# Performance work log

Hardware: AMD Instinct MI355X
Metric: run time of the kernel (lower is better)

The kernel has to match this reference:

```python
import jax, jax.numpy as jnp
import numpy as np

N = 50000; E = 800000; F_IN = 128; H = 16; G = 256
DIMS = [F_IN, H, 2 * H, 4 * H, 4 * H, 8 * H]
EPS = 1e-5


def setup_inputs() -> dict:
    key = jax.random.key(0)
    ks = iter(jax.random.split(key, 40))
    inp = {}
    inp["x"] = jax.random.normal(next(ks), (N, F_IN), dtype=jnp.float32)
    inp["edge_index"] = jax.random.randint(next(ks), (2, E), 0, N, dtype=jnp.int32)
    inp["edge_weight"] = jax.random.uniform(next(ks), (E,), dtype=jnp.float32)
    inp["batch"] = jnp.sort(jax.random.randint(next(ks), (N,), 0, G, dtype=jnp.int32))
    for i in range(5):
        din, dout = DIMS[i], DIMS[i + 1]
        inp[f"W{i+1}"] = jax.random.normal(next(ks), (din, dout), dtype=jnp.float32) / np.sqrt(din).astype(np.float32)
        inp[f"b{i+1}"] = jnp.zeros((dout,), jnp.float32)
        inp[f"g{i+1}"] = jnp.ones((dout,), jnp.float32)
        inp[f"bt{i+1}"] = jnp.zeros((dout,), jnp.float32)
    inp["fc1_w"] = jax.random.normal(next(ks), (8 * H, 4 * H), dtype=jnp.float32) / np.sqrt(8 * H).astype(np.float32)
    inp["fc1_b"] = jnp.zeros((4 * H,), jnp.float32)
    inp["fc2_w"] = jax.random.normal(next(ks), (4 * H, 1), dtype=jnp.float32) / np.sqrt(4 * H).astype(np.float32)
    inp["fc2_b"] = jnp.zeros((1,), jnp.float32)
    return inp


def _gcn_norm(edge_index, edge_weight, n):
    # PyG GCNConv: add self-loops (weight 1), symmetric deg^-1/2 normalization.
    loop = jnp.arange(n, dtype=edge_index.dtype)
    row = jnp.concatenate([edge_index[0], loop])  # source
    col = jnp.concatenate([edge_index[1], loop])  # target
    w = jnp.concatenate([edge_weight, jnp.ones((n,), edge_weight.dtype)])
    deg = jax.ops.segment_sum(w, col, num_segments=n)
    dis = jnp.where(deg > 0, jax.lax.rsqrt(jnp.maximum(deg, 1e-12)), 0.0)
    return row, col, dis[row] * w * dis[col]


def _bn(h, g, b):
    # BatchNorm1d, training-mode batch statistics (biased variance, eps=1e-5)
    mu = h.mean(0)
    v = h.var(0)
    return g * (h - mu) * jax.lax.rsqrt(v + EPS) + b


def reference(x, edge_index, edge_weight, batch,
              W1, b1, g1, bt1, W2, b2, g2, bt2, W3, b3, g3, bt3,
              W4, b4, g4, bt4, W5, b5, g5, bt5,
              fc1_w, fc1_b, fc2_w, fc2_b):
    n = x.shape[0]
    row, col, norm = _gcn_norm(edge_index, edge_weight, n)

    def conv(h, W, b):
        m = h @ W                                   # [N, dout] dense transform
        agg = jax.ops.segment_sum(m[row] * norm[:, None], col, num_segments=n)
        return agg + b

    h = _bn(jax.nn.relu(conv(x, W1, b1)), g1, bt1)
    h = _bn(jax.nn.relu(conv(h, W2, b2)), g2, bt2)
    h = _bn(jax.nn.relu(conv(h, W3, b3)), g3, bt3)
    h = jax.nn.relu(_bn(conv(h, W4, b4), g4, bt4))   # layer4: conv->bn->relu
    h = _bn(conv(h, W5, b5), g5, bt5)                # layer5: conv->bn
    pooled = jax.ops.segment_sum(h, batch, num_segments=G)  # global_add_pool -> [G, 8H]
    p = jax.nn.relu(pooled)
    p = jax.nn.relu(p @ fc1_w + fc1_b)
    # dropout is identity in eval mode
    return (p @ fc2_w + fc2_b).reshape(-1)          # [G]
```

## Files before the change

### kernel.cpp

```cpp
#include <hip/hip_runtime.h>
#include <stdint.h>

#define NN 50000
#define NE 800000
#define NG 256
#define NBUCKET 16
#define PARTSZ (NBUCKET * 256)

#define NBKT 391
#define ABLK 391
#define ASLICE 2048
#define BCAP 2560

__device__ __forceinline__ float bf2f(unsigned short u) {
    return __uint_as_float(((unsigned)u) << 16);
}
__device__ __forceinline__ unsigned short f2bf(float f) {
    unsigned b = __float_as_uint(f);
    return (unsigned short)((b + 0x7FFF + ((b >> 16) & 1)) >> 16);
}

__global__ void kA1(const int* __restrict__ col, int* __restrict__ bb, float* part, int e) {
    __shared__ int cnt[NBKT];
    for (int j = threadIdx.x; j < NBKT; j += 256) cnt[j] = 0;
    for (int i = blockIdx.x * 256 + threadIdx.x; i < 5 * PARTSZ; i += ABLK * 256) part[i] = 0.f;
    __syncthreads();
    int start = blockIdx.x * ASLICE;
    int end = min(start + ASLICE, e);
    for (int i = start + threadIdx.x; i < end; i += 256)
        atomicAdd(&cnt[col[i] >> 7], 1);
    __syncthreads();
    for (int j = threadIdx.x; j < NBKT; j += 256) bb[blockIdx.x * NBKT + j] = cnt[j];
}

__global__ void kA2a(int* __restrict__ bb, int* __restrict__ totals) {
    __shared__ int v[ABLK];
    int k = blockIdx.x;
    for (int b = threadIdx.x; b < ABLK; b += 256) v[b] = bb[b * NBKT + k];
    __syncthreads();
    if (threadIdx.x == 0) {
        int run = 0;
        for (int b = 0; b < ABLK; ++b) { int t = v[b]; v[b] = run; run += t; }
        totals[k] = run;
    }
    __syncthreads();
    for (int b = threadIdx.x; b < ABLK; b += 256) bb[b * NBKT + k] = v[b];
}

__global__ void kA2b(const int* __restrict__ totals, int* __restrict__ bucketbase) {
    __shared__ int v[NBKT];
    for (int j = threadIdx.x; j < NBKT; j += 256) v[j] = totals[j];
    __syncthreads();
    if (threadIdx.x == 0) {
        int run = 0;
        for (int k = 0; k < NBKT; ++k) { int t = v[k]; v[k] = run; run += t; }
        bucketbase[NBKT] = run;
    }
    __syncthreads();
    for (int j = threadIdx.x; j < NBKT; j += 256) bucketbase[j] = v[j];
}

__global__ void kA3(const int* __restrict__ row, const int* __restrict__ col,
                    const float* __restrict__ ew, const int* __restrict__ bb,
                    const int* __restrict__ bucketbase, int2* __restrict__ staging, int e) {
    __shared__ int cur[NBKT];
    for (int j = threadIdx.x; j < NBKT; j += 256)
        cur[j] = bucketbase[j] + bb[blockIdx.x * NBKT + j];
    __syncthreads();
    int start = blockIdx.x * ASLICE;
    int end = min(start + ASLICE, e);
    for (int i = start + threadIdx.x; i < end; i += 256) {
        int c = col[i];
        int p = atomicAdd(&cur[c >> 7], 1);
        staging[p] = make_int2(row[i] | ((c & 127) << 16), __float_as_int(ew[i]));
    }
}

__global__ void __launch_bounds__(256) kB(const int* __restrict__ bucketbase,
                                          const int2* __restrict__ staging,
                                          int2* __restrict__ csr, int* __restrict__ ptr,
                                          float* __restrict__ dis, int n) {
    __shared__ int2 st[BCAP];
    __shared__ int2 outb[BCAP];
    __shared__ int hist[129];
    __shared__ int cur[128];
    int k = blockIdx.x, t = threadIdx.x;
    int base = bucketbase[k], cnt = bucketbase[k + 1] - base;
    int node0 = k << 7;
    int ncov = min(128, n - node0);
    if (t < 129) hist[t] = 0;
    __syncthreads();
    if (cnt <= BCAP) {
        for (int i = t; i < cnt; i += 256) {
            int2 v = staging[base + i];
            st[i] = v;
            atomicAdd(&hist[v.x >> 16], 1);
        }
        __syncthreads();
        if (t == 0) {
            int run = 0;
            for (int j = 0; j < 128; ++j) { int h = hist[j]; hist[j] = run; run += h; }
            hist[128] = run;
        }
        __syncthreads();
        if (t < 128) cur[t] = hist[t];
        if (t < ncov) ptr[node0 + t] = base + hist[t];
        __syncthreads();
        for (int i = t; i < cnt; i += 256) {
            int2 v = st[i];
            int j = v.x >> 16;
            int p = atomicAdd(&cur[j], 1);
            outb[p] = make_int2(v.x & 0xFFFF, v.y);
        }
        __syncthreads();
        for (int i = t; i < cnt; i += 256) csr[base + i] = outb[i];
        if (t < ncov) {
            float s = 1.f;
            int a = hist[t], b2 = hist[t + 1];
            for (int p = a; p < b2; ++p) s += __int_as_float(outb[p].y);
            dis[node0 + t] = rsqrtf(s);
        }
    } else {
        for (int i = t; i < cnt; i += 256) atomicAdd(&hist[staging[base + i].x >> 16], 1);
        __syncthreads();
        if (t == 0) {
            int run = 0;
            for (int j = 0; j < 128; ++j) { int h = hist[j]; hist[j] = run; run += h; }
            hist[128] = run;
        }
        __syncthreads();
        if (t < 128) cur[t] = hist[t];
        if (t < ncov) ptr[node0 + t] = base + hist[t];
        __syncthreads();
        for (int i = t; i < cnt; i += 256) {
            int2 v = staging[base + i];
            int j = v.x >> 16;
            int p = atomicAdd(&cur[j], 1);
            csr[base + p] = make_int2(v.x & 0xFFFF, v.y);
        }
        __threadfence_block();
        __syncthreads();
        if (t < ncov) {
            float s = 1.f;
            int a = hist[t], b2 = hist[t + 1];
            for (int p = a; p < b2; ++p) s += __int_as_float(csr[base + p].y);
            dis[node0 + t] = rsqrtf(s);
        }
    }
    if (k == gridDim.x - 1 && t == 0) ptr[n] = bucketbase[NBKT];
}

__global__ void k_gemm1(const float* __restrict__ h, const float* __restrict__ W,
                        float* __restrict__ m, int n) {
    __shared__ float Wl[128 * 16];
    int tid = threadIdx.x;
    for (int i = tid; i < 128 * 16 / 4; i += 256)
        ((float4*)Wl)[i] = ((const float4*)W)[i];
    __syncthreads();
    int jq = tid % 4, group = tid / 4;
    int node0 = (blockIdx.x * 64 + group) * 2;
    const float4* h4 = (const float4*)h;
    int hb[2]; bool val[2];
#pragma unroll
    for (int i = 0; i < 2; ++i) {
        int nd = node0 + i;
        val[i] = nd < n;
        hb[i] = (val[i] ? nd : n - 1) * 32;
    }
    float4 acc[2];
    acc[0] = {0,0,0,0}; acc[1] = {0,0,0,0};
#pragma unroll 4
    for (int k4 = 0; k4 < 32; ++k4) {
        const float* wb = &Wl[(k4 * 4) * 16 + jq * 4];
        float4 w0 = *(const float4*)(wb);
        float4 w1 = *(const float4*)(wb + 16);
        float4 w2 = *(const float4*)(wb + 32);
        float4 w3 = *(const float4*)(wb + 48);
#pragma unroll
        for (int i = 0; i < 2; ++i) {
            float4 hv = h4[hb[i] + k4];
            acc[i].x += hv.x*w0.x + hv.y*w1.x + hv.z*w2.x + hv.w*w3.x;
            acc[i].y += hv.x*w0.y + hv.y*w1.y + hv.z*w2.y + hv.w*w3.y;
            acc[i].z += hv.x*w0.z + hv.y*w1.z + hv.z*w2.z + hv.w*w3.z;
            acc[i].w += hv.x*w0.w + hv.y*w1.w + hv.z*w2.w + hv.w*w3.w;
        }
    }
#pragma unroll
    for (int i = 0; i < 2; ++i)
        if (val[i]) ((float4*)m)[(node0 + i) * 4 + jq] = acc[i];
}

__global__ void k_l1gather(const float* __restrict__ src, const int* __restrict__ ptr,
                           int2* __restrict__ csr, const float* __restrict__ dis,
                           const float* __restrict__ bias, float* __restrict__ partOut,
                           float* __restrict__ out, int n) {
    __shared__ float ls[16], lq[16];
    int tid = threadIdx.x;
    if (tid < 16) { ls[tid] = 0.f; lq[tid] = 0.f; }
    __syncthreads();
    int t = blockIdx.x * 256 + tid;
    int node = t >> 2;
    int l4 = t & 3;
    bool valid = node < n;
    int nc = valid ? node : n - 1;
    const float4* s4 = (const float4*)src;
    float dc = dis[nc];
    float w0 = dc * dc;
    float4 v = s4[nc * 4 + l4];
    float4 acc = { w0 * v.x, w0 * v.y, w0 * v.z, w0 * v.w };
    int p0 = ptr[nc], p1 = ptr[nc + 1];
    int p = p0;
    for (; p + 4 <= p1; p += 4) {
        int2 c0 = csr[p], c1 = csr[p+1], c2 = csr[p+2], c3 = csr[p+3];
        float e0 = dis[c0.x] * __int_as_float(c0.y) * dc;
        float e1 = dis[c1.x] * __int_as_float(c1.y) * dc;
        float e2 = dis[c2.x] * __int_as_float(c2.y) * dc;
        float e3 = dis[c3.x] * __int_as_float(c3.y) * dc;
        float4 u0 = s4[c0.x * 4 + l4];
        float4 u1 = s4[c1.x * 4 + l4];
        float4 u2 = s4[c2.x * 4 + l4];
        float4 u3 = s4[c3.x * 4 + l4];
        acc.x += e0*u0.x + e1*u1.x + e2*u2.x + e3*u3.x;
        acc.y += e0*u0.y + e1*u1.y + e2*u2.y + e3*u3.y;
        acc.z += e0*u0.z + e1*u1.z + e2*u2.z + e3*u3.z;
        acc.w += e0*u0.w + e1*u1.w + e2*u2.w + e3*u3.w;
        if (l4 == 0) {
            csr[p]   = make_int2(c0.x, __float_as_int(e0));
            csr[p+1] = make_int2(c1.x, __float_as_int(e1));
            csr[p+2] = make_int2(c2.x, __float_as_int(e2));
            csr[p+3] = make_int2(c3.x, __float_as_int(e3));
        }
    }
    for (; p < p1; ++p) {
        int2 ce = csr[p];
        float w = dis[ce.x] * __int_as_float(ce.y) * dc;
        float4 u = s4[ce.x * 4 + l4];
        acc.x += w*u.x; acc.y += w*u.y; acc.z += w*u.z; acc.w += w*u.w;
        if (l4 == 0) csr[p] = make_int2(ce.x, __float_as_int(w));
    }
    float4 b = ((const float4*)bias)[l4];
    acc.x = fmaxf(acc.x + b.x, 0.f);
    acc.y = fmaxf(acc.y + b.y, 0.f);
    acc.z = fmaxf(acc.z + b.z, 0.f);
    acc.w = fmaxf(acc.w + b.w, 0.f);
    if (valid) ((float4*)out)[nc * 4 + l4] = acc;
    float s0 = valid ? acc.x : 0.f, s1 = valid ? acc.y : 0.f;
    float s2 = valid ? acc.z : 0.f, s3 = valid ? acc.w : 0.f;
    float q0 = s0*s0, q1 = s1*s1, q2 = s2*s2, q3 = s3*s3;
    for (int off = 4; off < 64; off <<= 1) {
        s0 += __shfl_down(s0, off, 64); s1 += __shfl_down(s1, off, 64);
        s2 += __shfl_down(s2, off, 64); s3 += __shfl_down(s3, off, 64);
        q0 += __shfl_down(q0, off, 64); q1 += __shfl_down(q1, off, 64);
        q2 += __shfl_down(q2, off, 64); q3 += __shfl_down(q3, off, 64);
    }
    int lane = tid & 63;
    if (lane < 4) {
        atomicAdd(&ls[4*lane+0], s0); atomicAdd(&ls[4*lane+1], s1);
        atomicAdd(&ls[4*lane+2], s2); atomicAdd(&ls[4*lane+3], s3);
        atomicAdd(&lq[4*lane+0], q0); atomicAdd(&lq[4*lane+1], q1);
        atomicAdd(&lq[4*lane+2], q2); atomicAdd(&lq[4*lane+3], q3);
    }
    __syncthreads();
    int bkt = (blockIdx.x & (NBUCKET - 1)) * 256;
    if (tid < 16) {
        atomicAdd(&partOut[bkt + tid], ls[tid]);
        atomicAdd(&partOut[bkt + 128 + tid], lq[tid]);
    }
}

template <int D, int BF16>
__device__ __forceinline__ float4 load_row(const void* src, int node, int l4) {
    if (BF16) {
        const unsigned short* sb = (const unsigned short*)src;
        ushort4 r = *(const ushort4*)(sb + (size_t)node * D + (l4 << 2));
        float4 f;
        f.x = bf2f(r.x); f.y = bf2f(r.y); f.z = bf2f(r.z); f.w = bf2f(r.w);
        return f;
    } else {
        const float4* s4 = (const float4*)src;
        return s4[(size_t)node * (D / 4) + l4];
    }
}

template <int DIN, int DOUT, int EP, int POSTAFF, int PREAFF, int RELU,
          int BF16IN, int BF16OUT, int NPB>
__global__ void __launch_bounds__(256) k_fused(
        const void* __restrict__ src, const int* __restrict__ ptr,
        const int2* __restrict__ csr, const float* __restrict__ dis,
        const float* __restrict__ partIn, const float* __restrict__ gmv,
        const float* __restrict__ btv, const float* __restrict__ W,
        const float* __restrict__ bias, float* __restrict__ partOut,
        void* __restrict__ out, int n) {
    const int TPN1 = DIN / 4, LPN = TPN1 * EP, GN1 = 256 / LPN;
    const int TPN2 = DOUT / 4, G2 = 256 / TPN2;
    const int HS = DIN + 4;
    __shared__ float Wl[DIN * DOUT];
    __shared__ float hrow[NPB * HS];
    __shared__ float scs[DIN], shs[DIN];
    __shared__ float ls[DOUT], lq[DOUT];
    int tid = threadIdx.x;
    for (int i = tid; i < DIN * DOUT / 4; i += 256)
        ((float4*)Wl)[i] = ((const float4*)W)[i];
    if (tid < DIN) {
        float s = 0.f, q = 0.f;
#pragma unroll
        for (int b2 = 0; b2 < NBUCKET; ++b2) {
            s += partIn[b2 * 256 + tid];
            q += partIn[b2 * 256 + 128 + tid];
        }
        float mu = s / (float)n;
        float var = q / (float)n - mu * mu;
        float a = gmv[tid] * rsqrtf(var + 1e-5f);
        scs[tid] = a;
        shs[tid] = btv[tid] - mu * a;
    }
    if (tid < DOUT) { ls[tid] = 0.f; lq[tid] = 0.f; }
    __syncthreads();

    int nodebase = blockIdx.x * NPB;
    {
        int grp = tid / LPN, r = tid % LPN;
        int e0 = r / TPN1, l4 = r % TPN1;
        float4 sc = ((const float4*)scs)[l4];
        float4 sh = ((const float4*)shs)[l4];
#pragma unroll
        for (int pass = 0; pass < NPB / GN1; ++pass) {
            int nl = pass * GN1 + grp;
            int node = nodebase + nl;
            int nc = node < n ? node : n - 1;
            float4 acc = {0.f, 0.f, 0.f, 0.f};
            float sumw = 0.f;
            if (e0 == 0) {
                float d = dis[nc];
                float w0 = d * d;
                float4 v = load_row<DIN, BF16IN>(src, nc, l4);
                if (PREAFF) {
                    v.x = fmaxf(sc.x*v.x+sh.x, 0.f); v.y = fmaxf(sc.y*v.y+sh.y, 0.f);
                    v.z = fmaxf(sc.z*v.z+sh.z, 0.f); v.w = fmaxf(sc.w*v.w+sh.w, 0.f);
                }
                acc.x = w0*v.x; acc.y = w0*v.y; acc.z = w0*v.z; acc.w = w0*v.w;
                sumw = w0;
            }
            int p0 = ptr[nc], p1 = ptr[nc + 1];
            int p = p0 + e0;
            for (; p + 3 * EP < p1; p += 4 * EP) {
                int2 c0 = csr[p], c1 = csr[p + EP], c2 = csr[p + 2*EP], c3 = csr[p + 3*EP];
                float e0w = __int_as_float(c0.y), e1w = __int_as_float(c1.y);
                float e2w = __int_as_float(c2.y), e3w = __int_as_float(c3.y);
                float4 u0 = load_row<DIN, BF16IN>(src, c0.x, l4);
                float4 u1 = load_row<DIN, BF16IN>(src, c1.x, l4);
                float4 u2 = load_row<DIN, BF16IN>(src, c2.x, l4);
                float4 u3 = load_row<DIN, BF16IN>(src, c3.x, l4);
                if (PREAFF) {
                    u0.x = fmaxf(sc.x*u0.x+sh.x,0.f); u0.y = fmaxf(sc.y*u0.y+sh.y,0.f);
                    u0.z = fmaxf(sc.z*u0.z+sh.z,0.f); u0.w = fmaxf(sc.w*u0.w+sh.w,0.f);
                    u1.x = fmaxf(sc.x*u1.x+sh.x,0.f); u1.y = fmaxf(sc.y*u1.y+sh.y,0.f);
                    u1.z = fmaxf(sc.z*u1.z+sh.z,0.f); u1.w = fmaxf(sc.w*u1.w+sh.w,0.f);
                    u2.x = fmaxf(sc.x*u2.x+sh.x,0.f); u2.y = fmaxf(sc.y*u2.y+sh.y,0.f);
                    u2.z = fmaxf(sc.z*u2.z+sh.z,0.f); u2.w = fmaxf(sc.w*u2.w+sh.w,0.f);
                    u3.x = fmaxf(sc.x*u3.x+sh.x,0.f); u3.y = fmaxf(sc.y*u3.y+sh.y,0.f);
                    u3.z = fmaxf(sc.z*u3.z+sh.z,0.f); u3.w = fmaxf(sc.w*u3.w+sh.w,0.f);
                }
                acc.x += e0w*u0.x + e1w*u1.x + e2w*u2.x + e3w*u3.x;
                acc.y += e0w*u0.y + e1w*u1.y + e2w*u2.y + e3w*u3.y;
                acc.z += e0w*u0.z + e1w*u1.z + e2w*u2.z + e3w*u3.z;
                acc.w += e0w*u0.w + e1w*u1.w + e2w*u2.w + e3w*u3.w;
                if (POSTAFF) sumw += e0w + e1w + e2w + e3w;
            }
            for (; p < p1; p += EP) {
                int2 ce = csr[p];
                float w = __int_as_float(ce.y);
                float4 u = load_row<DIN, BF16IN>(src, ce.x, l4);
                if (PREAFF) {
                    u.x = fmaxf(sc.x*u.x+sh.x,0.f); u.y = fmaxf(sc.y*u.y+sh.y,0.f);
                    u.z = fmaxf(sc.z*u.z+sh.z,0.f); u.w = fmaxf(sc.w*u.w+sh.w,0.f);
                }
                acc.x += w*u.x; acc.y += w*u.y; acc.z += w*u.z; acc.w += w*u.w;
                if (POSTAFF) sumw += w;
            }
#pragma unroll
            for (int off = TPN1; off < LPN; off <<= 1) {
                acc.x += __shfl_xor(acc.x, off, 64);
                acc.y += __shfl_xor(acc.y, off, 64);
                acc.z += __shfl_xor(acc.z, off, 64);
                acc.w += __shfl_xor(acc.w, off, 64);
                if (POSTAFF) sumw += __shfl_xor(sumw, off, 64);
            }
            if (POSTAFF) {
                acc.x = sc.x * acc.x + sh.x * sumw;
                acc.y = sc.y * acc.y + sh.y * sumw;
                acc.z = sc.z * acc.z + sh.z * sumw;
                acc.w = sc.w * acc.w + sh.w * sumw;
            }
            if (e0 == 0) *(float4*)&hrow[nl * HS + (l4 << 2)] = acc;
        }
    }
    __syncthreads();
    {
        int jq = tid % TPN2, g2 = tid / TPN2;
        float4 bv = ((const float4*)bias)[jq];
        float4 sv = {0,0,0,0}, qv = {0,0,0,0};
        for (int nl = g2; nl < NPB; nl += G2) {
            int node = nodebase + nl;
            bool valid = node < n;
            float4 a = {0.f, 0.f, 0.f, 0.f};
#pragma unroll
            for (int k4 = 0; k4 < DIN / 4; ++k4) {
                float4 hv = *(const float4*)&hrow[nl * HS + (k4 << 2)];
                const float* wb = &Wl[(k4 * 4) * DOUT + jq * 4];
                float4 w0 = *(const float4*)(wb);
                float4 w1 = *(const float4*)(wb + DOUT);
                float4 w2 = *(const float4*)(wb + 2 * DOUT);
                float4 w3 = *(const float4*)(wb + 3 * DOUT);
                a.x += hv.x*w0.x + hv.y*w1.x + hv.z*w2.x + hv.w*w3.x;
                a.y += hv.x*w0.y + hv.y*w1.y + hv.z*w2.y + hv.w*w3.y;
                a.z += hv.x*w0.z + hv.y*w1.z + hv.z*w2.z + hv.w*w3.z;
                a.w += hv.x*w0.w + hv.y*w1.w + hv.z*w2.w + hv.w*w3.w;
            }
            a.x += bv.x; a.y += bv.y; a.z += bv.z; a.w += bv.w;
            if (RELU) {
                a.x = fmaxf(a.x, 0.f); a.y = fmaxf(a.y, 0.f);
                a.z = fmaxf(a.z, 0.f); a.w = fmaxf(a.w, 0.f);
            }
            if (valid) {
                if (BF16OUT) {
                    ushort4 o;
                    o.x = f2bf(a.x); o.y = f2bf(a.y); o.z = f2bf(a.z); o.w = f2bf(a.w);
                    *(ushort4*)((unsigned short*)out + (size_t)node * DOUT + (jq << 2)) = o;
                } else {
                    ((float4*)out)[(size_t)node * TPN2 + jq] = a;
                }
                sv.x += a.x; sv.y += a.y; sv.z += a.z; sv.w += a.w;
                qv.x += a.x*a.x; qv.y += a.y*a.y; qv.z += a.z*a.z; qv.w += a.w*a.w;
            }
        }
        for (int off = TPN2; off < 64; off <<= 1) {
            sv.x += __shfl_down(sv.x, off, 64); sv.y += __shfl_down(sv.y, off, 64);
            sv.z += __shfl_down(sv.z, off, 64); sv.w += __shfl_down(sv.w, off, 64);
            qv.x += __shfl_down(qv.x, off, 64); qv.y += __shfl_down(qv.y, off, 64);
            qv.z += __shfl_down(qv.z, off, 64); qv.w += __shfl_down(qv.w, off, 64);
        }
        int lane = tid & 63;
        if (lane < TPN2) {
            atomicAdd(&ls[4*lane+0], sv.x); atomicAdd(&ls[4*lane+1], sv.y);
            atomicAdd(&ls[4*lane+2], sv.z); atomicAdd(&ls[4*lane+3], sv.w);
            atomicAdd(&lq[4*lane+0], qv.x); atomicAdd(&lq[4*lane+1], qv.y);
            atomicAdd(&lq[4*lane+2], qv.z); atomicAdd(&lq[4*lane+3], qv.w);
        }
        __syncthreads();
        int bkt = (blockIdx.x & (NBUCKET - 1)) * 256;
        if (tid < DOUT) {
            atomicAdd(&partOut[bkt + tid], ls[tid]);
            atomicAdd(&partOut[bkt + 128 + tid], lq[tid]);
        }
    }
}

__global__ void k_poolhead(const float* __restrict__ h, const int* __restrict__ batch,
                           const float* __restrict__ partIn, const float* __restrict__ gmv,
                           const float* __restrict__ btv,
                           const float* __restrict__ fc1w, const float* __restrict__ fc1b,
                           const float* __restrict__ fc2w, const float* __restrict__ fc2b,
                           float* __restrict__ out, int n) {
    __shared__ float tmp[256];
    __shared__ float pl[128];
    __shared__ float scs[128], shs[128];
    int g = blockIdx.x;
    int tid = threadIdx.x;
    if (tid < 128) {
        float s = 0.f, q = 0.f;
#pragma unroll
        for (int b2 = 0; b2 < NBUCKET; ++b2) {
            s += partIn[b2 * 256 + tid];
            q += partIn[b2 * 256 + 128 + tid];
        }
        float mu = s / (float)n;
        float var = q / (float)n - mu * mu;
        float a = gmv[tid] * rsqrtf(var + 1e-5f);
        scs[tid] = a;
        shs[tid] = btv[tid] - mu * a;
    }
    int j = tid & 127, prt = tid >> 7;
    int a = 0, b = n;
    while (a < b) { int mid = (a + b) >> 1; if (batch[mid] < g) a = mid + 1; else b = mid; }
    int lo = a;
    b = n;
    while (a < b) { int mid = (a + b) >> 1; if (batch[mid] < g + 1) a = mid + 1; else b = mid; }
    int hi = a;

    float acc = 0.f;
    for (int node = lo + prt; node < hi; node += 2) acc += h[(long)node * 128 + j];
    tmp[tid] = acc;
    __syncthreads();
    if (tid < 128) {
        float cnt = (float)(hi - lo);
        float p = scs[tid] * (tmp[tid] + tmp[tid + 128]) + shs[tid] * cnt;
        pl[tid] = fmaxf(p, 0.f);
    }
    __syncthreads();
    if (tid < 64) {
        float v1 = fc1b[tid];
        for (int k = 0; k < 128; ++k) v1 += pl[k] * fc1w[k * 64 + tid];
        v1 = fmaxf(v1, 0.f);
        float v = v1 * fc2w[tid];
        for (int off = 32; off > 0; off >>= 1) v += __shfl_down(v, off, 64);
        if (tid == 0) out[g] = v + fc2b[0];
    }
}

extern "C" void kernel_launch(void* const* d_in, const int* in_sizes, int n_in,
                              void* d_out, int out_size, void* d_ws, size_t ws_size,
                              hipStream_t stream) {
    const float* x     = (const float*)d_in[0];
    const int*   ei    = (const int*)d_in[1];
    const float* ew    = (const float*)d_in[2];
    const int*   batch = (const int*)d_in[3];
    const float *W[5], *b[5], *gm[5], *bt[5];
    for (int i = 0; i < 5; ++i) {
        W[i]  = (const float*)d_in[4 + 4 * i];
        b[i]  = (const float*)d_in[5 + 4 * i];
        gm[i] = (const float*)d_in[6 + 4 * i];
        bt[i] = (const float*)d_in[7 + 4 * i];
    }
    const float* fc1w = (const float*)d_in[24];
    const float* fc1b = (const float*)d_in[25];
    const float* fc2w = (const float*)d_in[26];
    const float* fc2b = (const float*)d_in[27];
    float* out = (float*)d_out;

    char* wsb = (char*)d_ws;
    float* dis    = (float*)wsb;  wsb += sizeof(float) * NN;
    int*   ptr    = (int*)wsb;    wsb += sizeof(int) * (NN + 4);
    int*   bb     = (int*)wsb;    wsb += sizeof(int) * ABLK * NBKT;
    int*   totals = (int*)wsb;    wsb += sizeof(int) * (NBKT + 1);
    int*   bbase  = (int*)wsb;    wsb += sizeof(int) * (NBKT + 3);
    wsb = (char*)(((uintptr_t)wsb + 15) & ~(uintptr_t)15);
    int2*  staging= (int2*)wsb;   wsb += sizeof(int2) * NE;
    int2*  csr    = (int2*)wsb;   wsb += sizeof(int2) * NE;
    float* part   = (float*)wsb;  wsb += sizeof(float) * 5 * PARTSZ;
    unsigned short* bufB1 = (unsigned short*)wsb;  wsb += sizeof(unsigned short) * (size_t)NN * 64;
    unsigned short* bufB2 = (unsigned short*)wsb;  wsb += sizeof(unsigned short) * (size_t)NN * 64;
    float* buf1   = (float*)wsb;  wsb += sizeof(float) * (size_t)NN * 16;
    float* buf2   = (float*)wsb;  wsb += sizeof(float) * (size_t)NN * 128;

    const int* row = ei;
    const int* col = ei + NE;
    const int B = 256;
    const int NBF = (NN + 15) / 16;

    kA1<<<ABLK, B, 0, stream>>>(col, bb, part, NE);
    kA2a<<<NBKT, B, 0, stream>>>(bb, totals);
    kA2b<<<1, B, 0, stream>>>(totals, bbase);
    kA3<<<ABLK, B, 0, stream>>>(row, col, ew, bb, bbase, staging, NE);
    kB<<<NBKT, B, 0, stream>>>(bbase, staging, csr, ptr, dis, NN);

    k_gemm1<<<(NN + 127) / 128, B, 0, stream>>>(x, W[0], buf1, NN);
    k_l1gather<<<(NN * 4 + 255) / 256, B, 0, stream>>>(buf1, ptr, csr, dis,
                                                       b[0], part + 0 * PARTSZ, buf2, NN);

    k_fused<16, 32, 4, 1, 0, 1, 0, 1, 16><<<NBF, B, 0, stream>>>(
        buf2, ptr, csr, dis, part + 0 * PARTSZ, gm[0], bt[0],
        W[1], b[1], part + 1 * PARTSZ, bufB1, NN);
    k_fused<32, 64, 4, 1, 0, 1, 1, 1, 16><<<NBF, B, 0, stream>>>(
        bufB1, ptr, csr, dis, part + 1 * PARTSZ, gm[1], bt[1],
        W[2], b[2], part + 2 * PARTSZ, bufB2, NN);
    k_fused<64, 64, 4, 1, 0, 0, 1, 1, 16><<<NBF, B, 0, stream>>>(
        bufB2, ptr, csr, dis, part + 2 * PARTSZ, gm[2], bt[2],
        W[3], b[3], part + 3 * PARTSZ, bufB1, NN);
    k_fused<64, 128, 4, 0, 1, 0, 1, 0, 16><<<NBF, B, 0, stream>>>(
        bufB1, ptr, csr, dis, part + 3 * PARTSZ, gm[3], bt[3],
        W[4], b[4], part + 4 * PARTSZ, buf2, NN);

    k_poolhead<<<NG, B, 0, stream>>>(buf2, batch, part + 4 * PARTSZ, gm[4], bt[4],
                                     fc1w, fc1b, fc2w, fc2b, out, NN);
}
```

Baseline: 421.6 us.

## Split final layer into gather-then-GEMM kernels instead of fused kernel

Replaces the fused aggregate+transform kernel for layer 5 with two kernels. The first gathers neighbor rows of the 64-wide bf16 input, applying the previous layer's BN and ReLU on the fly, and writes a 64-wide fp32 aggregate. The second runs a dense 64x128 GEMM with W in shared memory, adds the bias and accumulates BN statistics. The split exploits linearity so the gather works on 64 features rather than 128 outputs. The cost is an extra fp32 intermediate round trip through memory and one more kernel launch.

```diff
diff --git a/kernel.cpp b/kernel.cpp
--- a/kernel.cpp
+++ b/kernel.cpp
@@ -456,6 +456,161 @@
     }
 }
 
+__global__ void k_gather5(const unsigned short* __restrict__ src, const int* __restrict__ ptr,
+                          const int2* __restrict__ csr, const float* __restrict__ dis,
+                          const float* __restrict__ partIn, const float* __restrict__ gmv,
+                          const float* __restrict__ btv, float* __restrict__ out, int n) {
+    const int TPN = 16, EP = 4, LPN = 64;
+    __shared__ float scs[64], shs[64];
+    int tid = threadIdx.x;
+    if (tid < 64) {
+        float s = 0.f, q = 0.f;
+#pragma unroll
+        for (int b2 = 0; b2 < NBUCKET; ++b2) {
+            s += partIn[b2 * 256 + tid];
+            q += partIn[b2 * 256 + 128 + tid];
+        }
+        float mu = s / (float)n;
+        float var = q / (float)n - mu * mu;
+        float a = gmv[tid] * rsqrtf(var + 1e-5f);
+        scs[tid] = a;
+        shs[tid] = btv[tid] - mu * a;
+    }
+    __syncthreads();
+    int t = blockIdx.x * 256 + tid;
+    int node = t / LPN;
+    int r = t - node * LPN;
+    int e0 = r / TPN;
+    int l4 = r - e0 * TPN;
+    bool valid = node < n;
+    int nc = valid ? node : n - 1;
+    float4 sc = ((const float4*)scs)[l4];
+    float4 sh = ((const float4*)shs)[l4];
+    float4 acc = {0.f, 0.f, 0.f, 0.f};
+    if (e0 == 0) {
+        float d = dis[nc];
+        float w0 = d * d;
+        float4 v = load_row<64, 1>(src, nc, l4);
+        v.x = fmaxf(sc.x*v.x+sh.x, 0.f); v.y = fmaxf(sc.y*v.y+sh.y, 0.f);
+        v.z = fmaxf(sc.z*v.z+sh.z, 0.f); v.w = fmaxf(sc.w*v.w+sh.w, 0.f);
+        acc.x = w0*v.x; acc.y = w0*v.y; acc.z = w0*v.z; acc.w = w0*v.w;
+    }
+    int p0 = ptr[nc], p1 = ptr[nc + 1];
+    int p = p0 + e0;
+    for (; p + 3 * EP < p1; p += 4 * EP) {
+        int2 c0 = csr[p], c1 = csr[p + EP], c2 = csr[p + 2*EP], c3 = csr[p + 3*EP];
+        float e0w = __int_as_float(c0.y), e1w = __int_as_float(c1.y);
+        float e2w = __int_as_float(c2.y), e3w = __int_as_float(c3.y);
+        float4 u0 = load_row<64, 1>(src, c0.x, l4);
+        float4 u1 = load_row<64, 1>(src, c1.x, l4);
+        float4 u2 = load_row<64, 1>(src, c2.x, l4);
+        float4 u3 = load_row<64, 1>(src, c3.x, l4);
+        u0.x = fmaxf(sc.x*u0.x+sh.x,0.f); u0.y = fmaxf(sc.y*u0.y+sh.y,0.f);
+        u0.z = fmaxf(sc.z*u0.z+sh.z,0.f); u0.w = fmaxf(sc.w*u0.w+sh.w,0.f);
+        u1.x = fmaxf(sc.x*u1.x+sh.x,0.f); u1.y = fmaxf(sc.y*u1.y+sh.y,0.f);
+        u1.z = fmaxf(sc.z*u1.z+sh.z,0.f); u1.w = fmaxf(sc.w*u1.w+sh.w,0.f);
+        u2.x = fmaxf(sc.x*u2.x+sh.x,0.f); u2.y = fmaxf(sc.y*u2.y+sh.y,0.f);
+        u2.z = fmaxf(sc.z*u2.z+sh.z,0.f); u2.w = fmaxf(sc.w*u2.w+sh.w,0.f);
+        u3.x = fmaxf(sc.x*u3.x+sh.x,0.f); u3.y = fmaxf(sc.y*u3.y+sh.y,0.f);
+        u3.z = fmaxf(sc.z*u3.z+sh.z,0.f); u3.w = fmaxf(sc.w*u3.w+sh.w,0.f);
+        acc.x += e0w*u0.x + e1w*u1.x + e2w*u2.x + e3w*u3.x;
+        acc.y += e0w*u0.y + e1w*u1.y + e2w*u2.y + e3w*u3.y;
+        acc.z += e0w*u0.z + e1w*u1.z + e2w*u2.z + e3w*u3.z;
+        acc.w += e0w*u0.w + e1w*u1.w + e2w*u2.w + e3w*u3.w;
+    }
+    for (; p < p1; p += EP) {
+        int2 ce = csr[p];
+        float w = __int_as_float(ce.y);
+        float4 u = load_row<64, 1>(src, ce.x, l4);
+        u.x = fmaxf(sc.x*u.x+sh.x,0.f); u.y = fmaxf(sc.y*u.y+sh.y,0.f);
+        u.z = fmaxf(sc.z*u.z+sh.z,0.f); u.w = fmaxf(sc.w*u.w+sh.w,0.f);
+        acc.x += w*u.x; acc.y += w*u.y; acc.z += w*u.z; acc.w += w*u.w;
+    }
+#pragma unroll
+    for (int off = TPN; off < LPN; off <<= 1) {
+        acc.x += __shfl_xor(acc.x, off, 64);
+        acc.y += __shfl_xor(acc.y, off, 64);
+        acc.z += __shfl_xor(acc.z, off, 64);
+        acc.w += __shfl_xor(acc.w, off, 64);
+    }
+    if (valid && e0 == 0) ((float4*)out)[nc * TPN + l4] = acc;
+}
+
+__global__ void k_gemm5(const float* __restrict__ h, const float* __restrict__ W,
+                        const float* __restrict__ bias, float* __restrict__ partOut,
+                        float* __restrict__ m, int n) {
+    const int TPN = 32, GPB = 8, NPT = 4;
+    __shared__ float Wl[64 * 128];
+    __shared__ float ls[128], lq[128];
+    int tid = threadIdx.x;
+    for (int i = tid; i < 64 * 128 / 4; i += 256)
+        ((float4*)Wl)[i] = ((const float4*)W)[i];
+    if (tid < 128) { ls[tid] = 0.f; lq[tid] = 0.f; }
+    __syncthreads();
+
+    int jq = tid % TPN;
+    int group = tid / TPN;
+    int node0 = (blockIdx.x * GPB + group) * NPT;
+    const float4* h4 = (const float4*)h;
+    int hb[NPT]; bool val[NPT];
+#pragma unroll
+    for (int i = 0; i < NPT; ++i) {
+        int nd = node0 + i;
+        val[i] = nd < n;
+        hb[i] = (val[i] ? nd : n - 1) * 16;
+    }
+    float4 acc[NPT];
+#pragma unroll
+    for (int i = 0; i < NPT; ++i) acc[i] = {0.f, 0.f, 0.f, 0.f};
+#pragma unroll 4
+    for (int k4 = 0; k4 < 16; ++k4) {
+        const float* wb = &Wl[(k4 * 4) * 128 + jq * 4];
+        float4 w0 = *(const float4*)(wb);
+        float4 w1 = *(const float4*)(wb + 128);
+        float4 w2 = *(const float4*)(wb + 256);
+        float4 w3 = *(const float4*)(wb + 384);
+#pragma unroll
+        for (int i = 0; i < NPT; ++i) {
+            float4 hv = h4[hb[i] + k4];
+            acc[i].x += hv.x*w0.x + hv.y*w1.x + hv.z*w2.x + hv.w*w3.x;
+            acc[i].y += hv.x*w0.y + hv.y*w1.y + hv.z*w2.y + hv.w*w3.y;
+            acc[i].z += hv.x*w0.z + hv.y*w1.z + hv.z*w2.z + hv.w*w3.z;
+            acc[i].w += hv.x*w0.w + hv.y*w1.w + hv.z*w2.w + hv.w*w3.w;
+        }
+    }
+    float4 bv = ((const float4*)bias)[jq];
+    float4 sv = {0,0,0,0}, qv = {0,0,0,0};
+#pragma unroll
+    for (int i = 0; i < NPT; ++i) {
+        float4 a = acc[i];
+        a.x += bv.x; a.y += bv.y; a.z += bv.z; a.w += bv.w;
+        if (val[i]) {
+            ((float4*)m)[(size_t)(node0 + i) * TPN + jq] = a;
+            sv.x += a.x; sv.y += a.y; sv.z += a.z; sv.w += a.w;
+            qv.x += a.x*a.x; qv.y += a.y*a.y; qv.z += a.z*a.z; qv.w += a.w*a.w;
+        }
+    }
+    for (int off = TPN; off < 64; off <<= 1) {
+        sv.x += __shfl_down(sv.x, off, 64); sv.y += __shfl_down(sv.y, off, 64);
+        sv.z += __shfl_down(sv.z, off, 64); sv.w += __shfl_down(sv.w, off, 64);
+        qv.x += __shfl_down(qv.x, off, 64); qv.y += __shfl_down(qv.y, off, 64);
+        qv.z += __shfl_down(qv.z, off, 64); qv.w += __shfl_down(qv.w, off, 64);
+    }
+    int lane = tid & 63;
+    if (lane < TPN) {
+        atomicAdd(&ls[4*lane+0], sv.x); atomicAdd(&ls[4*lane+1], sv.y);
+        atomicAdd(&ls[4*lane+2], sv.z); atomicAdd(&ls[4*lane+3], sv.w);
+        atomicAdd(&lq[4*lane+0], qv.x); atomicAdd(&lq[4*lane+1], qv.y);
+        atomicAdd(&lq[4*lane+2], qv.z); atomicAdd(&lq[4*lane+3], qv.w);
+    }
+    __syncthreads();
+    int bkt = (blockIdx.x & (NBUCKET - 1)) * 256;
+    if (tid < 128) {
+        atomicAdd(&partOut[bkt + tid], ls[tid]);
+        atomicAdd(&partOut[bkt + 128 + tid], lq[tid]);
+    }
+}
+
 __global__ void k_poolhead(const float* __restrict__ h, const int* __restrict__ batch,
                            const float* __restrict__ partIn, const float* __restrict__ gmv,
                            const float* __restrict__ btv,
@@ -540,7 +695,7 @@
     float* part   = (float*)wsb;  wsb += sizeof(float) * 5 * PARTSZ;
     unsigned short* bufB1 = (unsigned short*)wsb;  wsb += sizeof(unsigned short) * (size_t)NN * 64;
     unsigned short* bufB2 = (unsigned short*)wsb;  wsb += sizeof(unsigned short) * (size_t)NN * 64;
-    float* buf1   = (float*)wsb;  wsb += sizeof(float) * (size_t)NN * 16;
+    float* buf1   = (float*)wsb;  wsb += sizeof(float) * (size_t)NN * 64;
     float* buf2   = (float*)wsb;  wsb += sizeof(float) * (size_t)NN * 128;
 
     const int* row = ei;
@@ -567,9 +722,10 @@
     k_fused<64, 64, 4, 1, 0, 0, 1, 1, 16><<<NBF, B, 0, stream>>>(
         bufB2, ptr, csr, dis, part + 2 * PARTSZ, gm[2], bt[2],
         W[3], b[3], part + 3 * PARTSZ, bufB1, NN);
-    k_fused<64, 128, 4, 0, 1, 0, 1, 0, 16><<<NBF, B, 0, stream>>>(
-        bufB1, ptr, csr, dis, part + 3 * PARTSZ, gm[3], bt[3],
-        W[4], b[4], part + 4 * PARTSZ, buf2, NN);
+
+    k_gather5<<<(int)(((long)NN * 64 + 255) / 256), B, 0, stream>>>(
+        bufB1, ptr, csr, dis, part + 3 * PARTSZ, gm[3], bt[3], buf1, NN);
+    k_gemm5<<<(NN + 31) / 32, B, 0, stream>>>(buf1, W[4], b[4], part + 4 * PARTSZ, buf2, NN);
 
     k_poolhead<<<NG, B, 0, stream>>>(buf2, batch, part + 4 * PARTSZ, gm[4], bt[4],
                                      fc1w, fc1b, fc2w, fc2b, out, NN);
```

New measurement: 414.5 us. No clear change (-1.7%).
